# Performance work log

Hardware: AMD Instinct MI355X
Metric: run time of the kernel (lower is better)

Reference implementation:

```python
import jax, jax.numpy as jnp
import numpy as np

EPS = 1e-5

def layer_norm(x, g, b):
    mu = jnp.mean(x, axis=-1, keepdims=True)
    var = jnp.var(x, axis=-1, keepdims=True)
    return (x - mu) * jax.lax.rsqrt(var + EPS) * g + b

def setup_inputs() -> dict:
    key = jax.random.key(0)
    ks = jax.random.split(key, 12)
    B, N, D, H = 32, 577, 768, 12
    Dh = D // H
    hid = 4 * D
    s = lambda d: 1.0 / np.sqrt(d)
    return {
        "x": jax.random.normal(ks[0], (B, N, D), jnp.float32),
        "ln1_g": jnp.ones((D,), jnp.float32),
        "ln1_b": jnp.zeros((D,), jnp.float32),
        "ln2_g": jnp.ones((D,), jnp.float32),
        "ln2_b": jnp.zeros((D,), jnp.float32),
        "w_qkv": jax.random.normal(ks[1], (D, 3 * D), jnp.float32) * s(D),
        "b_qkv": jnp.zeros((3 * D,), jnp.float32),
        "w_proj": jax.random.normal(ks[2], (D, D), jnp.float32) * s(D),
        "b_proj": jnp.zeros((D,), jnp.float32),
        "w_fc1": jax.random.normal(ks[3], (D, hid), jnp.float32) * s(D),
        "b_fc1": jnp.zeros((hid,), jnp.float32),
        "w_fc2": jax.random.normal(ks[4], (hid, D), jnp.float32) * s(hid),
        "b_fc2": jnp.zeros((D,), jnp.float32),
    }

def reference(x, ln1_g, ln1_b, ln2_g, ln2_b, w_qkv, b_qkv, w_proj, b_proj,
              w_fc1, b_fc1, w_fc2, b_fc2):
    B, N, D = x.shape
    H = 12
    Dh = D // H
    scale = Dh ** -0.5
    # --- attention branch ---
    h = layer_norm(x, ln1_g, ln1_b)
    qkv = h @ w_qkv + b_qkv                      # [B, N, 3D]
    qkv = qkv.reshape(B, N, 3, H, Dh).transpose(2, 0, 3, 1, 4)  # [3, B, H, N, Dh]
    q, k, v = qkv[0], qkv[1], qkv[2]
    attn = jnp.einsum('bhnd,bhmd->bhnm', q, k) * scale  # [B, H, N, N]
    attn = jax.nn.softmax(attn, axis=-1)
    o = jnp.einsum('bhnm,bhmd->bhnd', attn, v)           # [B, H, N, Dh]
    o = o.transpose(0, 2, 1, 3).reshape(B, N, D)
    o = o @ w_proj + b_proj
    x = x + o
    # --- MLP branch ---
    h = layer_norm(x, ln2_g, ln2_b)
    h = jnp.clip(h @ w_fc1 + b_fc1, 0.0, 6.0)            # ReLU6
    h = h @ w_fc2 + b_fc2
    return x + h
```

## Files before the change

kernel.cpp:

```cpp
#include <hip/hip_runtime.h>
#include <math.h>


typedef unsigned short u16;
typedef _Float16 f16;
typedef __attribute__((ext_vector_type(8))) _Float16 f16x8;
typedef __attribute__((ext_vector_type(4))) float f32x4;

__device__ __forceinline__ u16 f2h(float x) {
    union { f16 h; u16 u; } cv;
    cv.h = (f16)x;
    return cv.u;
}
__device__ __forceinline__ float h2f(u16 b) {
    union { u16 u; f16 h; } cv;
    cv.u = b;
    return (float)cv.h;
}
__device__ __forceinline__ void load_lds16(const u16* g, void* l) {
    __builtin_amdgcn_global_load_lds(
        (const __attribute__((address_space(1))) void*)g,
        (__attribute__((address_space(3))) void*)l, 16, 0, 0);
}
__device__ __forceinline__ int xcd_swz(int lid, int nwg) {
    const int x = lid & 7, pos = lid >> 3;
    const int q = nwg >> 3, r = nwg & 7;
    return (x < r ? x * (q + 1) : r * (q + 1) + (x - r) * q) + pos;
}

__global__ __launch_bounds__(256)
void wprep_kernel(const float* __restrict__ W, u16* __restrict__ Th,
                  int K, int N)
{
    __shared__ float t[32][33];
    const int n0 = blockIdx.x * 32, k0 = blockIdx.y * 32;
    const int tr = threadIdx.x >> 3, tc4 = (threadIdx.x & 7) * 4;
    const float4 v = *(const float4*)&W[(size_t)(k0 + tr) * N + n0 + tc4];
    t[tr][tc4 + 0] = v.x; t[tr][tc4 + 1] = v.y;
    t[tr][tc4 + 2] = v.z; t[tr][tc4 + 3] = v.w;
    __syncthreads();
    ushort4 h;
    h.x = f2h(t[tc4 + 0][tr]);
    h.y = f2h(t[tc4 + 1][tr]);
    h.z = f2h(t[tc4 + 2][tr]);
    h.w = f2h(t[tc4 + 3][tr]);
    *(ushort4*)&Th[(size_t)(n0 + tr) * K + k0 + tc4] = h;
}

__global__ __launch_bounds__(256)
void ln_kernel(const float* __restrict__ x, const float* __restrict__ g,
               const float* __restrict__ beta, u16* __restrict__ oh, int pad)
{
    const int row = blockIdx.x;
    const int tid = threadIdx.x;
    const float* xr = x + (size_t)row * 768;
    const float v0 = xr[tid], v1 = xr[tid + 256], v2 = xr[tid + 512];
    float s  = v0 + v1 + v2;
    float ss = v0 * v0 + v1 * v1 + v2 * v2;
    #pragma unroll
    for (int off = 1; off < 64; off <<= 1) {
        s  += __shfl_xor(s, off);
        ss += __shfl_xor(ss, off);
    }
    __shared__ float redS[4], redQ[4];
    const int wid = tid >> 6;
    if ((tid & 63) == 0) { redS[wid] = s; redQ[wid] = ss; }
    __syncthreads();
    s  = redS[0] + redS[1] + redS[2] + redS[3];
    ss = redQ[0] + redQ[1] + redQ[2] + redQ[3];
    const float mean = s * (1.0f / 768.0f);
    const float var  = ss * (1.0f / 768.0f) - mean * mean;
    const float rstd = rsqrtf(var + 1e-5f);
    int row_p = row;
    if (pad) {
        const unsigned bb = (unsigned)row / 577u;
        row_p = (int)(bb * 640u + ((unsigned)row - bb * 577u));
    }
    u16* ohr = oh + (size_t)row_p * 768;
    #pragma unroll
    for (int u = 0; u < 3; ++u) {
        const int c = tid + u * 256;
        const float vv = (u == 0) ? v0 : (u == 1) ? v1 : v2;
        ohr[c] = f2h((vv - mean) * rstd * g[c] + beta[c]);
    }
}

template<int RELU6, int RES, int OMODE, int PADMAP>
__global__ __launch_bounds__(256)
void mfma_gemm(const u16* __restrict__ Ah, const u16* __restrict__ Bh,
               const float* __restrict__ bias, const float* res,
               float* Cf, u16* __restrict__ Ch,
               u16* __restrict__ Qh_, u16* __restrict__ Kh_,
               u16* __restrict__ Vth_,
               int M, int N, int K)
{
    __shared__ u16 lds[32768];

    const int tid  = threadIdx.x;
    const int wave = tid >> 6;
    const int lane = tid & 63;

    const int nwg = gridDim.x * gridDim.y;
    int lid = blockIdx.y * gridDim.x + blockIdx.x;
    lid = xcd_swz(lid, nwg);
    const int bm = (lid / gridDim.x) * 128;
    const int bn = (lid % gridDim.x) * 128;

    const int r0 = wave * 16 + (lane >> 2);
    const int r1 = 64 + r0;
    const int c  = lane & 3;
    const int kg0 = c ^ ((r0 >> 1) & 3);
    const int kg1 = c ^ ((r1 >> 1) & 3);

    const u16* pA0 = Ah + (size_t)(bm + r0) * K + 8 * kg0;
    const u16* pA1 = Ah + (size_t)(bm + r1) * K + 8 * kg1;
    const u16* pB0 = Bh + (size_t)(bn + r0) * K + 8 * kg0;
    const u16* pB1 = Bh + (size_t)(bn + r1) * K + 8 * kg1;

    char* ldsb = (char*)lds;
    char* dA0 = ldsb +     0 + wave * 1024;
    char* dA1 = ldsb +  4096 + wave * 1024;
    char* dB0 = ldsb +  8192 + wave * 1024;
    char* dB1 = ldsb + 12288 + wave * 1024;

    const int am0 = (wave >> 1) * 64;
    const int bn0 = (wave & 1) * 64;
    const int l15 = lane & 15;
    const int lg  = lane >> 4;

    f32x4 acc[4][4] = {};
    const int nk = K >> 5;

    #pragma unroll
    for (int s = 0; s < 3; ++s) {
        const int o = s << 14;
        load_lds16(pA0, dA0 + o); load_lds16(pA1, dA1 + o);
        load_lds16(pB0, dB0 + o); load_lds16(pB1, dB1 + o);
        pA0 += 32; pA1 += 32; pB0 += 32; pB1 += 32;
    }

    for (int ks = 0; ks < nk; ++ks) {
        if (ks + 2 < nk)      asm volatile("s_waitcnt vmcnt(8)" ::: "memory");
        else if (ks + 1 < nk) asm volatile("s_waitcnt vmcnt(4)" ::: "memory");
        else                  asm volatile("s_waitcnt vmcnt(0)" ::: "memory");
        __builtin_amdgcn_s_barrier();
        if (ks + 3 < nk) {
            const int o = ((ks + 3) & 3) << 14;
            load_lds16(pA0, dA0 + o); load_lds16(pA1, dA1 + o);
            load_lds16(pB0, dB0 + o); load_lds16(pB1, dB1 + o);
            pA0 += 32; pA1 += 32; pB0 += 32; pB1 += 32;
        }
        const u16* sA = lds + ((ks & 3) << 13);
        const u16* sB = sA + 4096;

        f16x8 ah[4];
        #pragma unroll
        for (int fm = 0; fm < 4; ++fm) {
            const int ar = am0 + fm * 16 + l15;
            const int ph = (lg ^ ((ar >> 1) & 3)) * 8;
            ah[fm] = *(const f16x8*)&sA[ar * 32 + ph];
        }
        #pragma unroll
        for (int fn = 0; fn < 4; ++fn) {
            const int br = bn0 + fn * 16 + l15;
            const int ph = (lg ^ ((br >> 1) & 3)) * 8;
            const f16x8 bh = *(const f16x8*)&sB[br * 32 + ph];
            #pragma unroll
            for (int fm = 0; fm < 4; ++fm)
                acc[fm][fn] = __builtin_amdgcn_mfma_f32_16x16x32_f16(
                    ah[fm], bh, acc[fm][fn], 0, 0, 0);
        }
    }

    if (OMODE == 2) {
        __syncthreads();
        const int s  = bn / 768;
        const int hh = ((bn + bn0) - s * 768) >> 6;
        const int gr0 = bm + am0;
        const int bb  = gr0 / 640;
        const int n0  = gr0 - bb * 640;
        u16* eph = lds + wave * 4352;
        #pragma unroll
        for (int fn = 0; fn < 4; ++fn) {
            const float bv = bias[bn + bn0 + fn * 16 + l15];
            #pragma unroll
            for (int fm = 0; fm < 4; ++fm) {
                const f32x4 v = acc[fm][fn];
                #pragma unroll
                for (int j = 0; j < 4; ++j) {
                    const float o = v[j] + bv;
                    const int idx = (s == 2)
                        ? (fn * 16 + l15) * 68 + fm * 16 + lg * 4 + j
                        : (fm * 16 + lg * 4 + j) * 68 + fn * 16 + l15;
                    eph[idx] = f2h(o);
                }
            }
        }
        __syncthreads();
        if (s == 2) {
            u16* dh = Vth_ + (size_t)(bb * 12 + hh) * 64 * 640 + n0 + lane;
            #pragma unroll 8
            for (int d = 0; d < 64; ++d)
                dh[(size_t)d * 640] = eph[d * 68 + lane];
        } else {
            u16* base = ((s == 0) ? Qh_ : Kh_) +
                        ((size_t)(bb * 12 + hh) * 640 + n0) * 64 + lane;
            #pragma unroll 8
            for (int rr = 0; rr < 64; ++rr)
                base[(size_t)rr * 64] = eph[rr * 68 + lane];
        }
    } else {
        #pragma unroll
        for (int fn = 0; fn < 4; ++fn) {
            const int cc = bn + bn0 + fn * 16 + l15;
            const float bv = bias[cc];
            #pragma unroll
            for (int fm = 0; fm < 4; ++fm) {
                const int rbase = bm + am0 + fm * 16 + lg * 4;
                const f32x4 v = acc[fm][fn];
                #pragma unroll
                for (int j = 0; j < 4; ++j) {
                    const int r = rbase + j;
                    if (PADMAP) {
                        const int bb = r / 640;
                        const int nn = r - bb * 640;
                        if (nn < 577) {
                            const size_t ro = (size_t)(bb * 577 + nn) * N + cc;
                            float o = v[j] + bv;
                            if (RELU6) o = fminf(fmaxf(o, 0.0f), 6.0f);
                            if (RES)   o += res[ro];
                            Cf[ro] = o;
                        }
                    } else if (r < M) {
                        float o = v[j] + bv;
                        if (RELU6) o = fminf(fmaxf(o, 0.0f), 6.0f);
                        if (RES)   o += res[(size_t)r * N + cc];
                        if (OMODE == 0) Cf[(size_t)r * N + cc] = o;
                        else            Ch[(size_t)r * N + cc] = f2h(o);
                    }
                }
            }
        }
    }
}

__global__ __launch_bounds__(256)
void attn_mfma(const u16* __restrict__ Qh, const u16* __restrict__ Kh,
               const u16* __restrict__ Vth, u16* __restrict__ Oh)
{
    constexpr int SEQ = 577, NP = 640;
    __shared__ u16 sK[2 * 4096], sV[2 * 4096];
    __shared__ u16 sPh[4][16 * 72];

    const int tid  = threadIdx.x;
    const int wave = tid >> 6;
    const int lane = tid & 63;
    const int l15 = lane & 15, lg = lane >> 4;

    const int nwg = gridDim.x * gridDim.y;
    int lid = blockIdx.y * gridDim.x + blockIdx.x;
    lid = xcd_swz(lid, nwg);
    const int q0 = (lid % gridDim.x) * 64;
    const int bh = lid / gridDim.x;

    const size_t qkBase = (size_t)bh * NP * 64;
    const size_t vBase  = (size_t)bh * 64 * NP;

    f16x8 qfh[2];
    {
        const size_t ro = qkBase + (size_t)(q0 + wave * 16 + l15) * 64;
        #pragma unroll
        for (int ks = 0; ks < 2; ++ks)
            qfh[ks] = *(const f16x8*)&Qh[ro + (ks * 4 + lg) * 8];
    }

    const int srow = lane >> 3;
    const int sc   = lane & 7;

    f32x4 oacc[4] = {};
    float mrun = -1e30f, lrun = 0.0f;
    constexpr int NT = 10;

    #pragma unroll
    for (int t = 0; t < 2; ++t) {
        const int row = wave * 16 + t * 8 + srow;
        const int lc  = sc ^ (row & 7);
        load_lds16(Kh + qkBase + (size_t)row * 64 + lc * 8,
                   (char*)sK + wave * 2048 + t * 1024);
        load_lds16(Vth + vBase + (size_t)row * NP + lc * 8,
                   (char*)sV + wave * 2048 + t * 1024);
    }
    __syncthreads();

    int cur = 0;
    for (int it = 0; it < NT; ++it) {
        const int kv0 = it * 64;
        if (it + 1 < NT) {
            const int nkv = kv0 + 64;
            const int o = (cur ^ 1) * 8192;
            #pragma unroll
            for (int t = 0; t < 2; ++t) {
                const int row = wave * 16 + t * 8 + srow;
                const int lc  = sc ^ (row & 7);
                load_lds16(Kh + qkBase + (size_t)(nkv + row) * 64 + lc * 8,
                           (char*)sK + o + wave * 2048 + t * 1024);
                load_lds16(Vth + vBase + (size_t)row * NP + nkv + lc * 8,
                           (char*)sV + o + wave * 2048 + t * 1024);
            }
        }
        const u16* sKc = sK + cur * 4096;
        const u16* sVc = sV + cur * 4096;

        f32x4 sacc[4] = {};
        __builtin_amdgcn_s_setprio(1);
        #pragma unroll
        for (int fkv = 0; fkv < 4; ++fkv) {
            const int row = fkv * 16 + l15;
            #pragma unroll
            for (int ks = 0; ks < 2; ++ks) {
                const int ph = ((ks * 4 + lg) ^ (row & 7)) * 8;
                const f16x8 kh = *(const f16x8*)&sKc[row * 64 + ph];
                sacc[fkv] = __builtin_amdgcn_mfma_f32_16x16x32_f16(
                    kh, qfh[ks], sacc[fkv], 0, 0, 0);
            }
        }
        __builtin_amdgcn_s_setprio(0);

        float p[4][4];
        float mt = -1e30f;
        const bool tail = (kv0 + 64 > SEQ);
        #pragma unroll
        for (int fkv = 0; fkv < 4; ++fkv)
            #pragma unroll
            for (int j = 0; j < 4; ++j) {
                float sv = sacc[fkv][j] * 0.125f;
                if (tail && (kv0 + fkv * 16 + lg * 4 + j >= SEQ)) sv = -1e30f;
                p[fkv][j] = sv;
                mt = fmaxf(mt, sv);
            }
        mt = fmaxf(mt, __shfl_xor(mt, 16));
        mt = fmaxf(mt, __shfl_xor(mt, 32));
        const float mnew = fmaxf(mrun, mt);
        const float corr = __expf(mrun - mnew);
        float rs = 0.0f;
        #pragma unroll
        for (int fkv = 0; fkv < 4; ++fkv)
            #pragma unroll
            for (int j = 0; j < 4; ++j) {
                p[fkv][j] = __expf(p[fkv][j] - mnew);
                rs += p[fkv][j];
            }
        rs += __shfl_xor(rs, 16);
        rs += __shfl_xor(rs, 32);
        lrun = lrun * corr + rs;
        mrun = mnew;
        #pragma unroll
        for (int fd = 0; fd < 4; ++fd)
            #pragma unroll
            for (int j = 0; j < 4; ++j) oacc[fd][j] *= corr;

        u16* phr = &sPh[wave][l15 * 72];
        #pragma unroll
        for (int fkv = 0; fkv < 4; ++fkv) {
            ushort4 hv;
            hv.x = f2h(p[fkv][0]);
            hv.y = f2h(p[fkv][1]);
            hv.z = f2h(p[fkv][2]);
            hv.w = f2h(p[fkv][3]);
            *(ushort4*)&phr[fkv * 16 + lg * 4] = hv;
        }

        __builtin_amdgcn_s_setprio(1);
        #pragma unroll
        for (int ks = 0; ks < 2; ++ks) {
            const f16x8 pbh = *(const f16x8*)&sPh[wave][l15 * 72 + (ks * 4 + lg) * 8];
            #pragma unroll
            for (int fd = 0; fd < 4; ++fd) {
                const int row = fd * 16 + l15;
                const int ph = ((ks * 4 + lg) ^ (row & 7)) * 8;
                const f16x8 vh = *(const f16x8*)&sVc[row * 64 + ph];
                oacc[fd] = __builtin_amdgcn_mfma_f32_16x16x32_f16(
                    vh, pbh, oacc[fd], 0, 0, 0);
            }
        }
        __builtin_amdgcn_s_setprio(0);

        __syncthreads();
        cur ^= 1;
    }

    const int q = q0 + wave * 16 + l15;
    if (q < SEQ) {
        const float inv = 1.0f / lrun;
        const int b = bh / 12, h = bh % 12;
        const size_t rowo = ((size_t)(b * 640 + q)) * 768 + h * 64;
        #pragma unroll
        for (int fd = 0; fd < 4; ++fd) {
            ushort4 hv;
            hv.x = f2h(oacc[fd][0] * inv);
            hv.y = f2h(oacc[fd][1] * inv);
            hv.z = f2h(oacc[fd][2] * inv);
            hv.w = f2h(oacc[fd][3] * inv);
            *(ushort4*)&Oh[rowo + fd * 16 + lg * 4] = hv;
        }
    }
}

extern "C" void kernel_launch(void* const* d_in, const int* in_sizes, int n_in,
                              void* d_out, int out_size, void* d_ws, size_t ws_size,
                              hipStream_t stream)
{
    const float* x      = (const float*)d_in[0];
    const float* ln1_g  = (const float*)d_in[1];
    const float* ln1_b  = (const float*)d_in[2];
    const float* ln2_g  = (const float*)d_in[3];
    const float* ln2_b  = (const float*)d_in[4];
    const float* w_qkv  = (const float*)d_in[5];
    const float* b_qkv  = (const float*)d_in[6];
    const float* w_proj = (const float*)d_in[7];
    const float* b_proj = (const float*)d_in[8];
    const float* w_fc1  = (const float*)d_in[9];
    const float* b_fc1  = (const float*)d_in[10];
    const float* w_fc2  = (const float*)d_in[11];
    const float* b_fc2  = (const float*)d_in[12];
    float* out = (float*)d_out;

    const int M  = 18464;
    const int Mq = 20480;

    char* p = (char*)d_ws;
    u16* Wqkv  = (u16*)p;    p += (size_t)2304 * 768 * 2;
    u16* Wproj = (u16*)p;    p += (size_t)768 * 768 * 2;
    u16* Wfc1  = (u16*)p;    p += (size_t)3072 * 768 * 2;
    u16* Wfc2  = (u16*)p;    p += (size_t)768 * 3072 * 2;
    u16* A_h = (u16*)p;      p += (size_t)Mq * 768 * 2;
    u16* Qh  = (u16*)p;      p += (size_t)384 * 640 * 64 * 2;
    u16* Kh  = (u16*)p;      p += (size_t)384 * 640 * 64 * 2;
    u16* Vth = (u16*)p;      p += (size_t)384 * 64 * 640 * 2;
    u16* fc1h = (u16*)p;     p += (size_t)18560 * 3072 * 2;

    wprep_kernel<<<dim3(72, 24),  256, 0, stream>>>(w_qkv,  Wqkv,  768, 2304);
    wprep_kernel<<<dim3(24, 24),  256, 0, stream>>>(w_proj, Wproj, 768, 768);
    wprep_kernel<<<dim3(96, 24),  256, 0, stream>>>(w_fc1,  Wfc1,  768, 3072);
    wprep_kernel<<<dim3(24, 96),  256, 0, stream>>>(w_fc2,  Wfc2,  3072, 768);

    ln_kernel<<<M, 256, 0, stream>>>(x, ln1_g, ln1_b, A_h, 1);
    mfma_gemm<0, 0, 2, 0><<<dim3(18, 160), 256, 0, stream>>>(
        A_h, Wqkv, b_qkv, nullptr, nullptr, nullptr,
        Qh, Kh, Vth, Mq, 2304, 768);
    attn_mfma<<<dim3(10, 384), 256, 0, stream>>>(Qh, Kh, Vth, A_h);
    mfma_gemm<0, 1, 0, 1><<<dim3(6, 160), 256, 0, stream>>>(
        A_h, Wproj, b_proj, x, out, nullptr,
        nullptr, nullptr, nullptr, Mq, 768, 768);
    ln_kernel<<<M, 256, 0, stream>>>(out, ln2_g, ln2_b, A_h, 0);
    mfma_gemm<1, 0, 1, 0><<<dim3(24, 145), 256, 0, stream>>>(
        A_h, Wfc1, b_fc1, nullptr, nullptr, fc1h,
        nullptr, nullptr, nullptr, M, 3072, 768);
    mfma_gemm<0, 1, 0, 0><<<dim3(6, 145), 256, 0, stream>>>(
        fc1h, Wfc2, b_fc2, out, out, nullptr,
        nullptr, nullptr, nullptr, M, 768, 3072);
}
```

Before: 649.5 us.

## Enlarge GEMM tiles to 256x256 with 8 waves and double-buffered BK=64

Rewrites the MFMA GEMM to use 256x256 output tiles computed by 512 threads (8 waves, each owning 128x64), with a K-step of 64 and two LDS stages instead of 128x128 tiles, BK=32 and a four-stage ring. The aim is more operand reuse per LDS load and fewer global reads per FLOP. The QKV scatter epilogue is split into two 64-row halves, and the fc1 buffer is padded to cover the larger row tiles. The cost is a 128KB LDS footprint that likely allows only one block per CU. It also waits for all loads (vmcnt(0)) every iteration, so load/compute overlap is shallower.

Result: faster. 598.4 us (-7.9%).

```diff
diff --git a/kernel.cpp b/kernel.cpp
--- a/kernel.cpp
+++ b/kernel.cpp
@@ -86,7 +86,7 @@
 }
 
 template<int RELU6, int RES, int OMODE, int PADMAP>
-__global__ __launch_bounds__(256)
+__global__ __launch_bounds__(512, 2)
 void mfma_gemm(const u16* __restrict__ Ah, const u16* __restrict__ Bh,
                const float* __restrict__ bias, const float* res,
                float* Cf, u16* __restrict__ Ch,
@@ -94,129 +94,134 @@
                u16* __restrict__ Vth_,
                int M, int N, int K)
 {
-    __shared__ u16 lds[32768];
+    __shared__ u16 lds[65536];
 
     const int tid  = threadIdx.x;
-    const int wave = tid >> 6;
+    const int wid  = tid >> 6;
     const int lane = tid & 63;
+    const int wr = wid >> 2;
+    const int wc = wid & 3;
 
     const int nwg = gridDim.x * gridDim.y;
     int lid = blockIdx.y * gridDim.x + blockIdx.x;
     lid = xcd_swz(lid, nwg);
-    const int bm = (lid / gridDim.x) * 128;
-    const int bn = (lid % gridDim.x) * 128;
-
-    const int r0 = wave * 16 + (lane >> 2);
-    const int r1 = 64 + r0;
-    const int c  = lane & 3;
-    const int kg0 = c ^ ((r0 >> 1) & 3);
-    const int kg1 = c ^ ((r1 >> 1) & 3);
-
-    const u16* pA0 = Ah + (size_t)(bm + r0) * K + 8 * kg0;
-    const u16* pA1 = Ah + (size_t)(bm + r1) * K + 8 * kg1;
-    const u16* pB0 = Bh + (size_t)(bn + r0) * K + 8 * kg0;
-    const u16* pB1 = Bh + (size_t)(bn + r1) * K + 8 * kg1;
-
+    const int bm = (lid / gridDim.x) * 256;
+    const int bn = (lid % gridDim.x) * 256;
+
+    const int trow = tid >> 3;
+    const int c    = tid & 7;
+    const u16* pA[4]; const u16* pB[4];
+    char* dA[4]; char* dB[4];
     char* ldsb = (char*)lds;
-    char* dA0 = ldsb +     0 + wave * 1024;
-    char* dA1 = ldsb +  4096 + wave * 1024;
-    char* dB0 = ldsb +  8192 + wave * 1024;
-    char* dB1 = ldsb + 12288 + wave * 1024;
-
-    const int am0 = (wave >> 1) * 64;
-    const int bn0 = (wave & 1) * 64;
+    #pragma unroll
+    for (int i = 0; i < 4; ++i) {
+        const int r = i * 64 + trow;
+        const int kg = c ^ (r & 7);
+        pA[i] = Ah + (size_t)(bm + r) * K + kg * 8;
+        pB[i] = Bh + (size_t)(bn + r) * K + kg * 8;
+        dA[i] = ldsb +         i * 8192 + wid * 1024;
+        dB[i] = ldsb + 32768 + i * 8192 + wid * 1024;
+    }
+
     const int l15 = lane & 15;
     const int lg  = lane >> 4;
 
-    f32x4 acc[4][4] = {};
-    const int nk = K >> 5;
+    f32x4 acc[8][4] = {};
+    const int np = K >> 6;
 
     #pragma unroll
-    for (int s = 0; s < 3; ++s) {
-        const int o = s << 14;
-        load_lds16(pA0, dA0 + o); load_lds16(pA1, dA1 + o);
-        load_lds16(pB0, dB0 + o); load_lds16(pB1, dB1 + o);
-        pA0 += 32; pA1 += 32; pB0 += 32; pB1 += 32;
-    }
-
-    for (int ks = 0; ks < nk; ++ks) {
-        if (ks + 2 < nk)      asm volatile("s_waitcnt vmcnt(8)" ::: "memory");
-        else if (ks + 1 < nk) asm volatile("s_waitcnt vmcnt(4)" ::: "memory");
-        else                  asm volatile("s_waitcnt vmcnt(0)" ::: "memory");
+    for (int i = 0; i < 4; ++i) {
+        load_lds16(pA[i], dA[i]); load_lds16(pB[i], dB[i]);
+        pA[i] += 64; pB[i] += 64;
+    }
+
+    int cur = 0;
+    for (int p = 0; p < np; ++p) {
+        asm volatile("s_waitcnt vmcnt(0)" ::: "memory");
         __builtin_amdgcn_s_barrier();
-        if (ks + 3 < nk) {
-            const int o = ((ks + 3) & 3) << 14;
-            load_lds16(pA0, dA0 + o); load_lds16(pA1, dA1 + o);
-            load_lds16(pB0, dB0 + o); load_lds16(pB1, dB1 + o);
-            pA0 += 32; pA1 += 32; pB0 += 32; pB1 += 32;
-        }
-        const u16* sA = lds + ((ks & 3) << 13);
-        const u16* sB = sA + 4096;
-
-        f16x8 ah[4];
-        #pragma unroll
-        for (int fm = 0; fm < 4; ++fm) {
-            const int ar = am0 + fm * 16 + l15;
-            const int ph = (lg ^ ((ar >> 1) & 3)) * 8;
-            ah[fm] = *(const f16x8*)&sA[ar * 32 + ph];
-        }
-        #pragma unroll
-        for (int fn = 0; fn < 4; ++fn) {
-            const int br = bn0 + fn * 16 + l15;
-            const int ph = (lg ^ ((br >> 1) & 3)) * 8;
-            const f16x8 bh = *(const f16x8*)&sB[br * 32 + ph];
-            #pragma unroll
-            for (int fm = 0; fm < 4; ++fm)
-                acc[fm][fn] = __builtin_amdgcn_mfma_f32_16x16x32_f16(
-                    ah[fm], bh, acc[fm][fn], 0, 0, 0);
-        }
+        if (p + 1 < np) {
+            const int o = (cur ^ 1) * 65536;
+            #pragma unroll
+            for (int i = 0; i < 4; ++i) {
+                load_lds16(pA[i], dA[i] + o); load_lds16(pB[i], dB[i] + o);
+                pA[i] += 64; pB[i] += 64;
+            }
+        }
+        const u16* sA = lds + cur * 32768;
+        const u16* sB = sA + 16384;
+
+        #pragma unroll
+        for (int ss = 0; ss < 2; ++ss) {
+            f16x8 ah[8];
+            #pragma unroll
+            for (int fm = 0; fm < 8; ++fm) {
+                const int ar = wr * 128 + fm * 16 + l15;
+                const int pc = (ss * 4 + lg) ^ (ar & 7);
+                ah[fm] = *(const f16x8*)&sA[ar * 64 + pc * 8];
+            }
+            #pragma unroll
+            for (int fn = 0; fn < 4; ++fn) {
+                const int br = wc * 64 + fn * 16 + l15;
+                const int pc = (ss * 4 + lg) ^ (br & 7);
+                const f16x8 bh = *(const f16x8*)&sB[br * 64 + pc * 8];
+                #pragma unroll
+                for (int fm = 0; fm < 8; ++fm)
+                    acc[fm][fn] = __builtin_amdgcn_mfma_f32_16x16x32_f16(
+                        ah[fm], bh, acc[fm][fn], 0, 0, 0);
+            }
+        }
+        cur ^= 1;
     }
 
     if (OMODE == 2) {
         __syncthreads();
         const int s  = bn / 768;
-        const int hh = ((bn + bn0) - s * 768) >> 6;
-        const int gr0 = bm + am0;
-        const int bb  = gr0 / 640;
-        const int n0  = gr0 - bb * 640;
-        u16* eph = lds + wave * 4352;
+        const int hh = ((bn + wc * 64) - s * 768) >> 6;
+        u16* eph = lds + wid * 4352;
+        #pragma unroll
+        for (int h = 0; h < 2; ++h) {
+            #pragma unroll
+            for (int fn = 0; fn < 4; ++fn) {
+                const float bv = bias[bn + wc * 64 + fn * 16 + l15];
+                #pragma unroll
+                for (int f2 = 0; f2 < 4; ++f2) {
+                    const f32x4 v = acc[h * 4 + f2][fn];
+                    #pragma unroll
+                    for (int j = 0; j < 4; ++j) {
+                        const float o = v[j] + bv;
+                        const int idx = (s == 2)
+                            ? (fn * 16 + l15) * 68 + f2 * 16 + lg * 4 + j
+                            : (f2 * 16 + lg * 4 + j) * 68 + fn * 16 + l15;
+                        eph[idx] = f2h(o);
+                    }
+                }
+            }
+            __syncthreads();
+            const int gr0 = bm + wr * 128 + h * 64;
+            const int bb  = gr0 / 640;
+            const int n0  = gr0 - bb * 640;
+            if (s == 2) {
+                u16* dh = Vth_ + (size_t)(bb * 12 + hh) * 64 * 640 + n0 + lane;
+                #pragma unroll 8
+                for (int d = 0; d < 64; ++d)
+                    dh[(size_t)d * 640] = eph[d * 68 + lane];
+            } else {
+                u16* base = ((s == 0) ? Qh_ : Kh_) +
+                            ((size_t)(bb * 12 + hh) * 640 + n0) * 64 + lane;
+                #pragma unroll 8
+                for (int rr = 0; rr < 64; ++rr)
+                    base[(size_t)rr * 64] = eph[rr * 68 + lane];
+            }
+            __syncthreads();
+        }
+    } else {
         #pragma unroll
         for (int fn = 0; fn < 4; ++fn) {
-            const float bv = bias[bn + bn0 + fn * 16 + l15];
-            #pragma unroll
-            for (int fm = 0; fm < 4; ++fm) {
-                const f32x4 v = acc[fm][fn];
-                #pragma unroll
-                for (int j = 0; j < 4; ++j) {
-                    const float o = v[j] + bv;
-                    const int idx = (s == 2)
-                        ? (fn * 16 + l15) * 68 + fm * 16 + lg * 4 + j
-                        : (fm * 16 + lg * 4 + j) * 68 + fn * 16 + l15;
-                    eph[idx] = f2h(o);
-                }
-            }
-        }
-        __syncthreads();
-        if (s == 2) {
-            u16* dh = Vth_ + (size_t)(bb * 12 + hh) * 64 * 640 + n0 + lane;
-            #pragma unroll 8
-            for (int d = 0; d < 64; ++d)
-                dh[(size_t)d * 640] = eph[d * 68 + lane];
-        } else {
-            u16* base = ((s == 0) ? Qh_ : Kh_) +
-                        ((size_t)(bb * 12 + hh) * 640 + n0) * 64 + lane;
-            #pragma unroll 8
-            for (int rr = 0; rr < 64; ++rr)
-                base[(size_t)rr * 64] = eph[rr * 68 + lane];
-        }
-    } else {
-        #pragma unroll
-        for (int fn = 0; fn < 4; ++fn) {
-            const int cc = bn + bn0 + fn * 16 + l15;
+            const int cc = bn + wc * 64 + fn * 16 + l15;
             const float bv = bias[cc];
             #pragma unroll
-            for (int fm = 0; fm < 4; ++fm) {
-                const int rbase = bm + am0 + fm * 16 + lg * 4;
+            for (int fm = 0; fm < 8; ++fm) {
+                const int rbase = bm + wr * 128 + fm * 16 + lg * 4;
                 const f32x4 v = acc[fm][fn];
                 #pragma unroll
                 for (int j = 0; j < 4; ++j) {
@@ -427,6 +432,7 @@
 
     const int M  = 18464;
     const int Mq = 20480;
+    const int Mf = 18688;
 
     char* p = (char*)d_ws;
     u16* Wqkv  = (u16*)p;    p += (size_t)2304 * 768 * 2;
@@ -437,7 +443,7 @@
     u16* Qh  = (u16*)p;      p += (size_t)384 * 640 * 64 * 2;
     u16* Kh  = (u16*)p;      p += (size_t)384 * 640 * 64 * 2;
     u16* Vth = (u16*)p;      p += (size_t)384 * 64 * 640 * 2;
-    u16* fc1h = (u16*)p;     p += (size_t)18560 * 3072 * 2;
+    u16* fc1h = (u16*)p;     p += (size_t)Mf * 3072 * 2;
 
     wprep_kernel<<<dim3(72, 24),  256, 0, stream>>>(w_qkv,  Wqkv,  768, 2304);
     wprep_kernel<<<dim3(24, 24),  256, 0, stream>>>(w_proj, Wproj, 768, 768);
@@ -445,18 +451,18 @@
     wprep_kernel<<<dim3(24, 96),  256, 0, stream>>>(w_fc2,  Wfc2,  3072, 768);
 
     ln_kernel<<<M, 256, 0, stream>>>(x, ln1_g, ln1_b, A_h, 1);
-    mfma_gemm<0, 0, 2, 0><<<dim3(18, 160), 256, 0, stream>>>(
+    mfma_gemm<0, 0, 2, 0><<<dim3(9, 80), 512, 0, stream>>>(
         A_h, Wqkv, b_qkv, nullptr, nullptr, nullptr,
         Qh, Kh, Vth, Mq, 2304, 768);
     attn_mfma<<<dim3(10, 384), 256, 0, stream>>>(Qh, Kh, Vth, A_h);
-    mfma_gemm<0, 1, 0, 1><<<dim3(6, 160), 256, 0, stream>>>(
+    mfma_gemm<0, 1, 0, 1><<<dim3(3, 80), 512, 0, stream>>>(
         A_h, Wproj, b_proj, x, out, nullptr,
         nullptr, nullptr, nullptr, Mq, 768, 768);
     ln_kernel<<<M, 256, 0, stream>>>(out, ln2_g, ln2_b, A_h, 0);
-    mfma_gemm<1, 0, 1, 0><<<dim3(24, 145), 256, 0, stream>>>(
+    mfma_gemm<1, 0, 1, 0><<<dim3(12, 73), 512, 0, stream>>>(
         A_h, Wfc1, b_fc1, nullptr, nullptr, fc1h,
         nullptr, nullptr, nullptr, M, 3072, 768);
-    mfma_gemm<0, 1, 0, 0><<<dim3(6, 145), 256, 0, stream>>>(
+    mfma_gemm<0, 1, 0, 0><<<dim3(3, 73), 512, 0, stream>>>(
         fc1h, Wfc2, b_fc2, out, out, nullptr,
         nullptr, nullptr, nullptr, M, 768, 3072);
 }
```
